# Optimization experiments

Hardware: AMD Instinct MI355X
Metric: run time of the kernel (lower is better)

The kernel has to match this reference:

```python
import jax, jax.numpy as jnp
import numpy as np

N = 100000
E = 1600000
D_IN = 64
HID = 64
OUT = 64


def _glorot(key, shape):
    lim = float(np.sqrt(6.0 / (shape[0] + shape[1])))
    return jax.random.uniform(key, shape, jnp.float32, -lim, lim)


def setup_inputs() -> dict:
    key = jax.random.key(0)
    ks = jax.random.split(key, 10)
    x = jax.random.normal(ks[0], (N, D_IN), jnp.float32)
    edge_index = jax.random.randint(ks[1], (2, E), 0, N, jnp.int64)
    return {
        "x": x,
        "edge_index": edge_index,
        # SAGEConv1: lin_l (neighbors, with bias), lin_r (root, no bias)
        "W1l": _glorot(ks[2], (D_IN, HID)),
        "b1": jnp.zeros((HID,), jnp.float32),
        "W1r": _glorot(ks[3], (D_IN, HID)),
        # SAGEConv2
        "W2l": _glorot(ks[4], (HID, OUT)),
        "b2": jnp.zeros((OUT,), jnp.float32),
        "W2r": _glorot(ks[5], (HID, OUT)),
        # final Linear
        "Wlin": _glorot(ks[6], (OUT, OUT)),
        "blin": jnp.zeros((OUT,), jnp.float32),
    }


def _sage_conv(x, edge_index, Wl, bl, Wr):
    src, dst = edge_index[0], edge_index[1]
    # gather neighbor features [E, d], scatter-sum into destination nodes
    nbr_sum = jax.ops.segment_sum(x[src], dst, num_segments=N)
    cnt = jax.ops.segment_sum(jnp.ones((src.shape[0],), x.dtype), dst, num_segments=N)
    nbr_mean = nbr_sum / jnp.maximum(cnt, 1.0)[:, None]
    return nbr_mean @ Wl + bl + x @ Wr


def reference(x, edge_index, W1l, b1, W1r, W2l, b2, W2r, Wlin, blin):
    h = jax.nn.elu(_sage_conv(x, edge_index, W1l, b1, W1r))
    h = jax.nn.elu(_sage_conv(h, edge_index, W2l, b2, W2r))
    return h @ Wlin + blin
```

## Files before the change

kernel.cpp:

```cpp
#include <hip/hip_runtime.h>
#include <hip/hip_fp16.h>
#include <cmath>

#define D 64
#define PA_EDGES 4096
#define BSHIFT 7
#define BNODES 128
#define MAXBUCK 1024
#define PB_CAP 4096

typedef _Float16 f16x8 __attribute__((ext_vector_type(8)));
typedef float f32x4 __attribute__((ext_vector_type(4)));

__global__ __launch_bounds__(256)
void bhist_kernel(const int* __restrict__ dst, int* __restrict__ bcnt, int E, int nbuck) {
    __shared__ int lh[MAXBUCK];
    const int t = threadIdx.x;
    const int e0 = blockIdx.x * PA_EDGES;
    const int ecnt = min(PA_EDGES, E - e0);
    for (int i = t; i < MAXBUCK; i += 256) lh[i] = 0;
    __syncthreads();
    for (int i = t; i < ecnt; i += 256) atomicAdd(&lh[dst[e0 + i] >> BSHIFT], 1);
    __syncthreads();
    for (int b = t; b < nbuck; b += 256) {
        const int c = lh[b];
        if (c) atomicAdd(&bcnt[b], c);
    }
}

__global__ __launch_bounds__(256)
void bucket_scan_kernel(const int* __restrict__ bcnt, int* __restrict__ bbase,
                        int* __restrict__ cursor, int nbuck, int E) {
    __shared__ int red[256];
    const int t = threadIdx.x;
    const int c0 = (4 * t + 0 < nbuck) ? bcnt[4 * t + 0] : 0;
    const int c1 = (4 * t + 1 < nbuck) ? bcnt[4 * t + 1] : 0;
    const int c2 = (4 * t + 2 < nbuck) ? bcnt[4 * t + 2] : 0;
    const int c3 = (4 * t + 3 < nbuck) ? bcnt[4 * t + 3] : 0;
    red[t] = c0 + c1 + c2 + c3;
    __syncthreads();
    for (int off = 1; off < 256; off <<= 1) {
        int u = (t >= off) ? red[t - off] : 0;
        __syncthreads();
        red[t] += u;
        __syncthreads();
    }
    const int excl = (t == 0) ? 0 : red[t - 1];
    const int e0 = excl, e1 = excl + c0, e2 = excl + c0 + c1, e3 = excl + c0 + c1 + c2;
    if (4 * t + 0 <= nbuck) { bbase[4 * t + 0] = e0; }
    if (4 * t + 1 <= nbuck) { bbase[4 * t + 1] = e1; }
    if (4 * t + 2 <= nbuck) { bbase[4 * t + 2] = e2; }
    if (4 * t + 3 <= nbuck) { bbase[4 * t + 3] = e3; }
    if (4 * t + 0 < nbuck) cursor[4 * t + 0] = e0;
    if (4 * t + 1 < nbuck) cursor[4 * t + 1] = e1;
    if (4 * t + 2 < nbuck) cursor[4 * t + 2] = e2;
    if (4 * t + 3 < nbuck) cursor[4 * t + 3] = e3;
    if (t == 255) bbase[nbuck] = E;
}

__global__ __launch_bounds__(256)
void partition_kernel(const int* __restrict__ src, const int* __restrict__ dst,
                      int* __restrict__ cursor, unsigned* __restrict__ pairs,
                      int E, int nbuck) {
    __shared__ int lhist[MAXBUCK];
    __shared__ int lbase[MAXBUCK];
    __shared__ int gbase[MAXBUCK];
    __shared__ int red[256];
    __shared__ unsigned stage[PA_EDGES];
    __shared__ unsigned short sbuck[PA_EDGES];

    const int t = threadIdx.x;
    const int e0 = blockIdx.x * PA_EDGES;
    const int ecnt = min(PA_EDGES, E - e0);

    for (int i = t; i < MAXBUCK; i += 256) lhist[i] = 0;
    __syncthreads();
    for (int i = t; i < ecnt; i += 256) atomicAdd(&lhist[dst[e0 + i] >> BSHIFT], 1);
    __syncthreads();

    const int c0 = lhist[4 * t], c1 = lhist[4 * t + 1];
    const int c2 = lhist[4 * t + 2], c3 = lhist[4 * t + 3];
    red[t] = c0 + c1 + c2 + c3;
    __syncthreads();
    for (int off = 1; off < 256; off <<= 1) {
        int u = (t >= off) ? red[t - off] : 0;
        __syncthreads();
        red[t] += u;
        __syncthreads();
    }
    const int excl = (t == 0) ? 0 : red[t - 1];
    lbase[4 * t]     = excl;
    lbase[4 * t + 1] = excl + c0;
    lbase[4 * t + 2] = excl + c0 + c1;
    lbase[4 * t + 3] = excl + c0 + c1 + c2;
    for (int b = t; b < nbuck; b += 256) {
        const int c = lhist[b];
        gbase[b] = c ? atomicAdd(&cursor[b], c) : 0;
    }
    __syncthreads();
    for (int i = t; i < MAXBUCK; i += 256) lhist[i] = 0;
    __syncthreads();
    for (int i = t; i < ecnt; i += 256) {
        const int d = dst[e0 + i];
        const int b = d >> BSHIFT;
        const int p = lbase[b] + atomicAdd(&lhist[b], 1);
        stage[p] = ((unsigned)src[e0 + i] << BSHIFT) | (unsigned)(d & (BNODES - 1));
        sbuck[p] = (unsigned short)b;
    }
    __syncthreads();
    for (int i = t; i < ecnt; i += 256) {
        const int b = sbuck[i];
        pairs[gbase[b] + (i - lbase[b])] = stage[i];
    }
}

__global__ __launch_bounds__(256)
void bucket_fill_kernel(const unsigned* __restrict__ pairs, const int* __restrict__ bbase,
                        int* __restrict__ rowStart, int* __restrict__ csr, int n, int E) {
    __shared__ int lcsr[PB_CAP];
    __shared__ int lcnt[BNODES];
    __shared__ int lrs[BNODES];
    __shared__ int s[BNODES];
    __shared__ int lfill[BNODES];
    const int t = threadIdx.x;
    const int node0 = blockIdx.x << BSHIFT;
    const int bn = min(BNODES, n - node0);
    const int base = bbase[blockIdx.x];
    const int cntE = bbase[blockIdx.x + 1] - base;

    if (t < BNODES) { lcnt[t] = 0; lfill[t] = 0; }
    __syncthreads();
    for (int i = t; i < cntE; i += 256)
        atomicAdd(&lcnt[pairs[base + i] & (BNODES - 1)], 1);
    __syncthreads();
    if (t < BNODES) s[t] = lcnt[t];
    __syncthreads();
    for (int off = 1; off < BNODES; off <<= 1) {
        int u = (t >= off && t < BNODES) ? s[t - off] : 0;
        __syncthreads();
        if (t < BNODES) s[t] += u;
        __syncthreads();
    }
    if (t < BNODES) lrs[t] = (t == 0) ? 0 : s[t - 1];
    __syncthreads();
    if (t < bn) rowStart[node0 + t] = base + lrs[t];
    if (blockIdx.x == gridDim.x - 1 && t == 0) rowStart[n] = E;

    if (cntE <= PB_CAP) {
        for (int i = t; i < cntE; i += 256) {
            const unsigned pr = pairs[base + i];
            const int dl = (int)(pr & (BNODES - 1));
            const int p = lrs[dl] + atomicAdd(&lfill[dl], 1);
            lcsr[p] = (int)(pr >> BSHIFT);
        }
        __syncthreads();
        for (int i = t; i < cntE; i += 256) csr[base + i] = lcsr[i];
    } else {
        for (int i = t; i < cntE; i += 256) {
            const unsigned pr = pairs[base + i];
            const int dl = (int)(pr & (BNODES - 1));
            const int p = base + lrs[dl] + atomicAdd(&lfill[dl], 1);
            csr[p] = (int)(pr >> BSHIFT);
        }
    }
}

__global__ __launch_bounds__(256)
void cast_half_kernel(const float* __restrict__ in, __half* __restrict__ out, int n2) {
    const float2* in2 = (const float2*)in;
    __half2* out2 = (__half2*)out;
    int i = blockIdx.x * 256 + threadIdx.x;
    const int st = gridDim.x * 256;
    for (; i < n2; i += st) {
        const float2 v = in2[i];
        out2[i] = __floats2half2_rn(v.x, v.y);
    }
}

__global__ __launch_bounds__(256)
void pack_wb_kernel(const float* __restrict__ W1l, const float* __restrict__ W1r,
                    const float* __restrict__ W2l, const float* __restrict__ W2r,
                    const float* __restrict__ Wlin, __half* __restrict__ wB) {
    const int t = blockIdx.x * 256 + threadIdx.x;
    if (t >= 5 * 4096) return;
    const int mat = t >> 12;
    const float* W = (mat == 0) ? W1l : (mat == 1) ? W1r : (mat == 2) ? W2l
                    : (mat == 3) ? W2r : Wlin;
    const int r = t & 4095;
    const int e = r & 7;
    const int ln = (r >> 3) & 63;
    const int kk = (r >> 9) & 1;
    const int c = r >> 10;
    const int k = kk * 32 + ((ln >> 4) << 3) + e;
    const int col = c * 16 + (ln & 15);
    wB[t] = __float2half_rn(W[k * D + col]);
}

__device__ __forceinline__ void addh4(float4& a, const __half* __restrict__ p) {
    union { unsigned long long u; __half2 h[2]; } r;
    r.u = *(const unsigned long long*)p;
    const float2 f0 = __half22float2(r.h[0]);
    const float2 f1 = __half22float2(r.h[1]);
    a.x += f0.x; a.y += f0.y; a.z += f1.x; a.w += f1.y;
}

__global__ __launch_bounds__(256)
void aggmean_kernel(const __half* __restrict__ xh, const int* __restrict__ rowStart,
                    const int* __restrict__ csr, __half* __restrict__ m, int n) {
    const int lane = threadIdx.x & 63;
    const int g = lane >> 4;
    const int gl = lane & 15;
    const int wave = threadIdx.x >> 6;
    const int gw = blockIdx.x * 4 + wave;
    const int nw = gridDim.x * 4;

    for (int node = gw; node < n; node += nw) {
        const int r0 = rowStart[node];
        const int r1 = rowStart[node + 1];
        float4 acc0 = make_float4(0.f, 0.f, 0.f, 0.f);
        float4 acc1 = make_float4(0.f, 0.f, 0.f, 0.f);

        int j = r0;
        for (; j + 16 <= r1; j += 16) {
            const int i0 = csr[j + 0  + g];
            const int i1 = csr[j + 4  + g];
            const int i2 = csr[j + 8  + g];
            const int i3 = csr[j + 12 + g];
            addh4(acc0, &xh[(size_t)i0 * D + gl * 4]);
            addh4(acc1, &xh[(size_t)i1 * D + gl * 4]);
            addh4(acc0, &xh[(size_t)i2 * D + gl * 4]);
            addh4(acc1, &xh[(size_t)i3 * D + gl * 4]);
        }
        const int rem = r1 - j;
        if (rem > 0) {
            if (0 + g < rem) {
                const int sidx = csr[j + 0 + g];
                addh4(acc0, &xh[(size_t)sidx * D + gl * 4]);
            }
            if (4 + g < rem) {
                const int sidx = csr[j + 4 + g];
                addh4(acc1, &xh[(size_t)sidx * D + gl * 4]);
            }
            if (8 + g < rem) {
                const int sidx = csr[j + 8 + g];
                addh4(acc0, &xh[(size_t)sidx * D + gl * 4]);
            }
            if (12 + g < rem) {
                const int sidx = csr[j + 12 + g];
                addh4(acc1, &xh[(size_t)sidx * D + gl * 4]);
            }
        }

        float4 a;
        a.x = acc0.x + acc1.x; a.y = acc0.y + acc1.y;
        a.z = acc0.z + acc1.z; a.w = acc0.w + acc1.w;
        a.x += __shfl_xor(a.x, 16); a.y += __shfl_xor(a.y, 16);
        a.z += __shfl_xor(a.z, 16); a.w += __shfl_xor(a.w, 16);
        a.x += __shfl_xor(a.x, 32); a.y += __shfl_xor(a.y, 32);
        a.z += __shfl_xor(a.z, 32); a.w += __shfl_xor(a.w, 32);

        if (lane < 16) {
            const float rdeg = 1.0f / fmaxf((float)(r1 - r0), 1.0f);
            const __half2 p0 = __floats2half2_rn(a.x * rdeg, a.y * rdeg);
            const __half2 p1 = __floats2half2_rn(a.z * rdeg, a.w * rdeg);
            uint2 o = make_uint2(__builtin_bit_cast(unsigned, p0),
                                 __builtin_bit_cast(unsigned, p1));
            ((uint2*)m)[(size_t)node * 16 + gl] = o;
        }
    }
}

__global__ __launch_bounds__(256)
void mm_layer_kernel(const __half* __restrict__ mh,
                     const __half* __restrict__ res,
                     const __half* __restrict__ wA,
                     const float* __restrict__ ba,
                     const __half* __restrict__ wB,
                     __half* __restrict__ hout,
                     int n) {
    const int lane = threadIdx.x & 63;
    const int wave = threadIdx.x >> 6;
    const int g = blockIdx.x * 4 + wave;
    const int node0 = g * 16;
    if (node0 >= n) return;
    const int li = lane & 15, hi = lane >> 4;

    const int nodeA = min(node0 + li, n - 1);
    const f16x8 am0 = *(const f16x8*)&mh[(size_t)nodeA * D + hi * 8];
    const f16x8 am1 = *(const f16x8*)&mh[(size_t)nodeA * D + 32 + hi * 8];
    const f16x8 ax0 = *(const f16x8*)&res[(size_t)nodeA * D + hi * 8];
    const f16x8 ax1 = *(const f16x8*)&res[(size_t)nodeA * D + 32 + hi * 8];

#pragma unroll
    for (int c = 0; c < 4; ++c) {
        const f16x8 bA0 = *(const f16x8*)&wA[((c * 2 + 0) * 64 + lane) * 8];
        const f16x8 bA1 = *(const f16x8*)&wA[((c * 2 + 1) * 64 + lane) * 8];
        const f16x8 bB0 = *(const f16x8*)&wB[((c * 2 + 0) * 64 + lane) * 8];
        const f16x8 bB1 = *(const f16x8*)&wB[((c * 2 + 1) * 64 + lane) * 8];
        const float bv = ba[c * 16 + li];
        f32x4 acc = {bv, bv, bv, bv};
        acc = __builtin_amdgcn_mfma_f32_16x16x32_f16(am0, bA0, acc, 0, 0, 0);
        acc = __builtin_amdgcn_mfma_f32_16x16x32_f16(am1, bA1, acc, 0, 0, 0);
        acc = __builtin_amdgcn_mfma_f32_16x16x32_f16(ax0, bB0, acc, 0, 0, 0);
        acc = __builtin_amdgcn_mfma_f32_16x16x32_f16(ax1, bB1, acc, 0, 0, 0);
#pragma unroll
        for (int r = 0; r < 4; ++r) {
            float v = acc[r];
            v = v > 0.0f ? v : expm1f(v);
            const float vp = __shfl_xor(v, 1);
            const int noder = node0 + hi * 4 + r;
            if (!(lane & 1) && noder < n) {
                const __half2 p = __floats2half2_rn(v, vp);
                *(__half2*)&hout[(size_t)noder * D + c * 16 + li] = p;
            }
        }
    }
}

__global__ __launch_bounds__(256)
void mm_final_kernel(const __half* __restrict__ h,
                     const __half* __restrict__ wF,
                     const float* __restrict__ bias,
                     float* __restrict__ out,
                     int n) {
    const int lane = threadIdx.x & 63;
    const int wave = threadIdx.x >> 6;
    const int g = blockIdx.x * 4 + wave;
    const int node0 = g * 16;
    if (node0 >= n) return;
    const int li = lane & 15, hi = lane >> 4;

    const int nodeA = min(node0 + li, n - 1);
    const f16x8 ah0 = *(const f16x8*)&h[(size_t)nodeA * D + hi * 8];
    const f16x8 ah1 = *(const f16x8*)&h[(size_t)nodeA * D + 32 + hi * 8];

#pragma unroll
    for (int c = 0; c < 4; ++c) {
        const f16x8 b0 = *(const f16x8*)&wF[((c * 2 + 0) * 64 + lane) * 8];
        const f16x8 b1 = *(const f16x8*)&wF[((c * 2 + 1) * 64 + lane) * 8];
        const float bv = bias[c * 16 + li];
        f32x4 acc = {bv, bv, bv, bv};
        acc = __builtin_amdgcn_mfma_f32_16x16x32_f16(ah0, b0, acc, 0, 0, 0);
        acc = __builtin_amdgcn_mfma_f32_16x16x32_f16(ah1, b1, acc, 0, 0, 0);
#pragma unroll
        for (int r = 0; r < 4; ++r) {
            const int noder = node0 + hi * 4 + r;
            if (noder < n)
                out[(size_t)noder * D + c * 16 + li] = acc[r];
        }
    }
}

extern "C" void kernel_launch(void* const* d_in, const int* in_sizes, int n_in,
                              void* d_out, int out_size, void* d_ws, size_t ws_size,
                              hipStream_t stream) {
    const float* x    = (const float*)d_in[0];
    const int*   ei   = (const int*)d_in[1];
    const float* W1l  = (const float*)d_in[2];
    const float* b1   = (const float*)d_in[3];
    const float* W1r  = (const float*)d_in[4];
    const float* W2l  = (const float*)d_in[5];
    const float* b2   = (const float*)d_in[6];
    const float* W2r  = (const float*)d_in[7];
    const float* Wlin = (const float*)d_in[8];
    const float* blin = (const float*)d_in[9];

    const int N_ = in_sizes[0] / D;
    const int E_ = in_sizes[1] / 2;
    const int* src = ei;
    const int* dst = ei + E_;

    int* bcnt     = (int*)d_ws;
    int* bbase    = bcnt + MAXBUCK;
    int* cursor   = bbase + MAXBUCK + 1;
    int* rowStart = cursor + MAXBUCK;
    unsigned* pairs = (unsigned*)(rowStart + N_ + 1);
    int* csr      = (int*)(pairs + E_);
    uintptr_t pa = (uintptr_t)(csr + E_);
    pa = (pa + 63) & ~(uintptr_t)63;
    __half* wBbuf = (__half*)pa;
    __half* mh    = wBbuf + 5 * 4096;
    __half* fh    = mh + (size_t)N_ * D;

    const __half* wb1l  = wBbuf;
    const __half* wb1r  = wBbuf + 4096;
    const __half* wb2l  = wBbuf + 8192;
    const __half* wb2r  = wBbuf + 12288;
    const __half* wblin = wBbuf + 16384;

    const int nbuck = (N_ + BNODES - 1) >> BSHIFT;
    const int npart = (E_ + PA_EDGES - 1) / PA_EDGES;
    const int ngrp  = (N_ + 15) / 16;
    const int gmm   = (ngrp + 3) / 4;

    hipMemsetAsync(bcnt, 0, (size_t)MAXBUCK * sizeof(int), stream);

    bhist_kernel<<<npart, 256, 0, stream>>>(dst, bcnt, E_, nbuck);
    bucket_scan_kernel<<<1, 256, 0, stream>>>(bcnt, bbase, cursor, nbuck, E_);
    partition_kernel<<<npart, 256, 0, stream>>>(src, dst, cursor, pairs, E_, nbuck);
    bucket_fill_kernel<<<nbuck, 256, 0, stream>>>(pairs, bbase, rowStart, csr, N_, E_);
    cast_half_kernel<<<1024, 256, 0, stream>>>(x, fh, N_ * D / 2);
    pack_wb_kernel<<<(5 * 4096 + 255) / 256, 256, 0, stream>>>(
        W1l, W1r, W2l, W2r, Wlin, wBbuf);

    aggmean_kernel<<<2048, 256, 0, stream>>>(fh, rowStart, csr, mh, N_);
    mm_layer_kernel<<<gmm, 256, 0, stream>>>(mh, fh, wb1l, b1, wb1r, fh, N_);
    aggmean_kernel<<<2048, 256, 0, stream>>>(fh, rowStart, csr, mh, N_);
    mm_layer_kernel<<<gmm, 256, 0, stream>>>(mh, fh, wb2l, b2, wb2r, fh, N_);
    mm_final_kernel<<<gmm, 256, 0, stream>>>(fh, wblin, blin, (float*)d_out, N_);
}
```

Baseline: 209.0 us.

## Fuse final linear into layer-2 matmul and merge cast with weight packing

The final Linear is folded into the second SAGE layer kernel. The ELU output goes into a swizzled per-wave LDS tile and is multiplied by Wlin in the same kernel, so the fp16 hidden state is no longer written to and reread from global memory. Separately, the x-to-half cast and the weight packing now run in one launch instead of two. The fused path relies on same-wave LDS visibility with no barrier, and the final kernel's lane-to-data mapping must match the layout written to LDS.

```diff
diff --git a/kernel.cpp b/kernel.cpp
--- a/kernel.cpp
+++ b/kernel.cpp
@@ -166,34 +166,31 @@
 }
 
 __global__ __launch_bounds__(256)
-void cast_half_kernel(const float* __restrict__ in, __half* __restrict__ out, int n2) {
+void cast_pack_kernel(const float* __restrict__ in, __half* __restrict__ out, int n2,
+                      const float* __restrict__ W1l, const float* __restrict__ W1r,
+                      const float* __restrict__ W2l, const float* __restrict__ W2r,
+                      const float* __restrict__ Wlin, __half* __restrict__ wB) {
+    const int gid = blockIdx.x * 256 + threadIdx.x;
+    if (gid < 5 * 4096) {
+        const int mat = gid >> 12;
+        const float* W = (mat == 0) ? W1l : (mat == 1) ? W1r : (mat == 2) ? W2l
+                        : (mat == 3) ? W2r : Wlin;
+        const int r = gid & 4095;
+        const int e = r & 7;
+        const int ln = (r >> 3) & 63;
+        const int kk = (r >> 9) & 1;
+        const int c = r >> 10;
+        const int k = kk * 32 + ((ln >> 4) << 3) + e;
+        const int col = c * 16 + (ln & 15);
+        wB[gid] = __float2half_rn(W[k * D + col]);
+    }
     const float2* in2 = (const float2*)in;
     __half2* out2 = (__half2*)out;
-    int i = blockIdx.x * 256 + threadIdx.x;
     const int st = gridDim.x * 256;
-    for (; i < n2; i += st) {
+    for (int i = gid; i < n2; i += st) {
         const float2 v = in2[i];
         out2[i] = __floats2half2_rn(v.x, v.y);
     }
-}
-
-__global__ __launch_bounds__(256)
-void pack_wb_kernel(const float* __restrict__ W1l, const float* __restrict__ W1r,
-                    const float* __restrict__ W2l, const float* __restrict__ W2r,
-                    const float* __restrict__ Wlin, __half* __restrict__ wB) {
-    const int t = blockIdx.x * 256 + threadIdx.x;
-    if (t >= 5 * 4096) return;
-    const int mat = t >> 12;
-    const float* W = (mat == 0) ? W1l : (mat == 1) ? W1r : (mat == 2) ? W2l
-                    : (mat == 3) ? W2r : Wlin;
-    const int r = t & 4095;
-    const int e = r & 7;
-    const int ln = (r >> 3) & 63;
-    const int kk = (r >> 9) & 1;
-    const int c = r >> 10;
-    const int k = kk * 32 + ((ln >> 4) << 3) + e;
-    const int col = c * 16 + (ln & 15);
-    wB[t] = __float2half_rn(W[k * D + col]);
 }
 
 __device__ __forceinline__ void addh4(float4& a, const __half* __restrict__ p) {
@@ -270,20 +267,26 @@
     }
 }
 
+template <bool FINAL>
 __global__ __launch_bounds__(256)
 void mm_layer_kernel(const __half* __restrict__ mh,
                      const __half* __restrict__ res,
                      const __half* __restrict__ wA,
                      const float* __restrict__ ba,
                      const __half* __restrict__ wB,
+                     const __half* __restrict__ wF,
+                     const float* __restrict__ bfin,
                      __half* __restrict__ hout,
+                     float* __restrict__ fout,
                      int n) {
+    __shared__ __half lt[FINAL ? 4 * 16 * 64 : 4];
     const int lane = threadIdx.x & 63;
     const int wave = threadIdx.x >> 6;
     const int g = blockIdx.x * 4 + wave;
     const int node0 = g * 16;
     if (node0 >= n) return;
     const int li = lane & 15, hi = lane >> 4;
+    char* wtile = (char*)&lt[wave * 16 * 64];
 
     const int nodeA = min(node0 + li, n - 1);
     const f16x8 am0 = *(const f16x8*)&mh[(size_t)nodeA * D + hi * 8];
@@ -308,45 +311,41 @@
             float v = acc[r];
             v = v > 0.0f ? v : expm1f(v);
             const float vp = __shfl_xor(v, 1);
-            const int noder = node0 + hi * 4 + r;
-            if (!(lane & 1) && noder < n) {
-                const __half2 p = __floats2half2_rn(v, vp);
-                *(__half2*)&hout[(size_t)noder * D + c * 16 + li] = p;
-            }
-        }
-    }
-}
-
-__global__ __launch_bounds__(256)
-void mm_final_kernel(const __half* __restrict__ h,
-                     const __half* __restrict__ wF,
-                     const float* __restrict__ bias,
-                     float* __restrict__ out,
-                     int n) {
-    const int lane = threadIdx.x & 63;
-    const int wave = threadIdx.x >> 6;
-    const int g = blockIdx.x * 4 + wave;
-    const int node0 = g * 16;
-    if (node0 >= n) return;
-    const int li = lane & 15, hi = lane >> 4;
-
-    const int nodeA = min(node0 + li, n - 1);
-    const f16x8 ah0 = *(const f16x8*)&h[(size_t)nodeA * D + hi * 8];
-    const f16x8 ah1 = *(const f16x8*)&h[(size_t)nodeA * D + 32 + hi * 8];
-
+            if (!FINAL) {
+                const int noder = node0 + hi * 4 + r;
+                if (!(lane & 1) && noder < n) {
+                    const __half2 p = __floats2half2_rn(v, vp);
+                    *(__half2*)&hout[(size_t)noder * D + c * 16 + li] = p;
+                }
+            } else {
+                if (!(lane & 1)) {
+                    const int row = hi * 4 + r;
+                    const int boff = (c * 32 + li * 2) ^ ((row & 7) << 4);
+                    *(__half2*)(wtile + row * 128 + boff) = __floats2half2_rn(v, vp);
+                }
+            }
+        }
+    }
+
+    if (FINAL) {
+        const int row = li;
+        const int sw = (row & 7);
+        const f16x8 ah0 = *(const f16x8*)(wtile + row * 128 + ((hi ^ sw) << 4));
+        const f16x8 ah1 = *(const f16x8*)(wtile + row * 128 + (((4 + hi) ^ sw) << 4));
 #pragma unroll
-    for (int c = 0; c < 4; ++c) {
-        const f16x8 b0 = *(const f16x8*)&wF[((c * 2 + 0) * 64 + lane) * 8];
-        const f16x8 b1 = *(const f16x8*)&wF[((c * 2 + 1) * 64 + lane) * 8];
-        const float bv = bias[c * 16 + li];
-        f32x4 acc = {bv, bv, bv, bv};
-        acc = __builtin_amdgcn_mfma_f32_16x16x32_f16(ah0, b0, acc, 0, 0, 0);
-        acc = __builtin_amdgcn_mfma_f32_16x16x32_f16(ah1, b1, acc, 0, 0, 0);
+        for (int c = 0; c < 4; ++c) {
+            const f16x8 b0 = *(const f16x8*)&wF[((c * 2 + 0) * 64 + lane) * 8];
+            const f16x8 b1 = *(const f16x8*)&wF[((c * 2 + 1) * 64 + lane) * 8];
+            const float bv = bfin[c * 16 + li];
+            f32x4 acc = {bv, bv, bv, bv};
+            acc = __builtin_amdgcn_mfma_f32_16x16x32_f16(ah0, b0, acc, 0, 0, 0);
+            acc = __builtin_amdgcn_mfma_f32_16x16x32_f16(ah1, b1, acc, 0, 0, 0);
 #pragma unroll
-        for (int r = 0; r < 4; ++r) {
-            const int noder = node0 + hi * 4 + r;
-            if (noder < n)
-                out[(size_t)noder * D + c * 16 + li] = acc[r];
+            for (int r = 0; r < 4; ++r) {
+                const int noder = node0 + hi * 4 + r;
+                if (noder < n)
+                    fout[(size_t)noder * D + c * 16 + li] = acc[r];
+            }
         }
     }
 }
@@ -399,13 +398,13 @@
     bucket_scan_kernel<<<1, 256, 0, stream>>>(bcnt, bbase, cursor, nbuck, E_);
     partition_kernel<<<npart, 256, 0, stream>>>(src, dst, cursor, pairs, E_, nbuck);
     bucket_fill_kernel<<<nbuck, 256, 0, stream>>>(pairs, bbase, rowStart, csr, N_, E_);
-    cast_half_kernel<<<1024, 256, 0, stream>>>(x, fh, N_ * D / 2);
-    pack_wb_kernel<<<(5 * 4096 + 255) / 256, 256, 0, stream>>>(
-        W1l, W1r, W2l, W2r, Wlin, wBbuf);
+    cast_pack_kernel<<<1024, 256, 0, stream>>>(x, fh, N_ * D / 2,
+                                               W1l, W1r, W2l, W2r, Wlin, wBbuf);
 
     aggmean_kernel<<<2048, 256, 0, stream>>>(fh, rowStart, csr, mh, N_);
-    mm_layer_kernel<<<gmm, 256, 0, stream>>>(mh, fh, wb1l, b1, wb1r, fh, N_);
+    mm_layer_kernel<false><<<gmm, 256, 0, stream>>>(
+        mh, fh, wb1l, b1, wb1r, nullptr, nullptr, fh, nullptr, N_);
     aggmean_kernel<<<2048, 256, 0, stream>>>(fh, rowStart, csr, mh, N_);
-    mm_layer_kernel<<<gmm, 256, 0, stream>>>(mh, fh, wb2l, b2, wb2r, fh, N_);
-    mm_final_kernel<<<gmm, 256, 0, stream>>>(fh, wblin, blin, (float*)d_out, N_);
-}
+    mm_layer_kernel<true><<<gmm, 256, 0, stream>>>(
+        mh, fh, wb2l, b2, wb2r, wblin, blin, nullptr, (float*)d_out, N_);
+}
```

After: 201.2 us. 3.7% less time.
